# Performance work log

Hardware: AMD Instinct MI355X
Metric: run time of the kernel (lower is better)

Reference implementation:

```python
import jax, jax.numpy as jnp
import numpy as np

CONTEXT = 10  # symmetric_mask default; self.context is NOT used in call()
SCALE = 16.0  # hard-coded divisor in the source
NEG = 1e9


def setup_inputs() -> dict:
    key = jax.random.key(0)
    k1, k2, k3, k4 = jax.random.split(key, 4)
    B, N, D = 2, 4096, 512
    H, dh = 8, 64
    x = jax.random.normal(k1, (B, N, D), dtype=jnp.float32)
    Wq = jax.random.normal(k2, (H, D, dh), dtype=jnp.float32) * 1e-4
    Wv = jax.random.normal(k3, (H, D, dh), dtype=jnp.float32) * 1e-4
    Wup = jax.random.normal(k4, (H * dh, D), dtype=jnp.float32) * 1e-4
    return {"x": x, "Wq": Wq, "Wv": Wv, "Wup": Wup}


def reference(x, Wq, Wv, Wup):
    B, N, D = x.shape
    H, _, dh = Wq.shape
    # Per-head projections (no bias), vectorized over heads
    Q = jnp.einsum('bnd,hdk->bhnk', x, Wq)  # [B,H,N,dh]
    V = jnp.einsum('bnd,hdk->bhnk', x, Wv)  # [B,H,N,dh]
    # Full score matrix Q @ V^T / 16 (V doubles as keys in this module)
    scores = jnp.einsum('bhnk,bhmk->bhnm', Q, V) / SCALE  # [B,H,N,N]
    # Symmetric band mask: |i-j| <= CONTEXT and |i-j| > 0 (diagonal excluded)
    idx = jnp.arange(N)
    diff = jnp.abs(idx[:, None] - idx[None, :])
    mask = (diff <= CONTEXT) & (diff > 0)  # [N,N]
    scores = scores - NEG * (~mask).astype(scores.dtype)
    weights = jax.nn.softmax(scores, axis=-1)
    C = jnp.einsum('bhnm,bhmk->bhnk', weights, V)  # [B,H,N,dh]
    heads = C.transpose(0, 2, 1, 3).reshape(B, N, H * dh)  # concat heads
    return heads @ Wup  # [B,N,D]
```

## Files before the change

### kernel.cpp

```cpp
#include <hip/hip_runtime.h>
#include <math.h>

#define N_TOK 4096
#define DMODEL 512
#define NHEAD 8
#define DHEAD 64
#define CTX 10
#define NROW 8192

typedef __bf16 bf16x8 __attribute__((ext_vector_type(8)));
typedef float  f32x4  __attribute__((ext_vector_type(4)));

#define GLOAD_LDS16(g, l) __builtin_amdgcn_global_load_lds(                 \
    (const __attribute__((address_space(1))) void*)(g),                     \
    (__attribute__((address_space(3))) void*)(l), 16, 0, 0)

__global__ __launch_bounds__(256) void conv_x(const float* __restrict__ x,
                                              __bf16* __restrict__ xb)
{
    const int idx = (blockIdx.x * 256 + threadIdx.x) * 8;
    const float4 a = *(const float4*)(x + idx);
    const float4 b = *(const float4*)(x + idx + 4);
    bf16x8 o;
    o[0] = (__bf16)a.x; o[1] = (__bf16)a.y; o[2] = (__bf16)a.z; o[3] = (__bf16)a.w;
    o[4] = (__bf16)b.x; o[5] = (__bf16)b.y; o[6] = (__bf16)b.z; o[7] = (__bf16)b.w;
    *(bf16x8*)(xb + idx) = o;
}

__global__ __launch_bounds__(256) void conv_wqv(const float* __restrict__ Wq,
                                                const float* __restrict__ Wv,
                                                __bf16* __restrict__ Wt)
{
    __shared__ float T[64][65];
    const int k0  = blockIdx.x * 64;
    const int h   = blockIdx.y;
    const int mat = blockIdx.z;
    const float* src = (mat ? Wv : Wq) + (size_t)h * DMODEL * DHEAD;
    const int tid = threadIdx.x;
#pragma unroll
    for (int it = 0; it < 4; it++) {
        const int kr = it * 16 + (tid >> 4);
        const int c4 = (tid & 15) * 4;
        const float4 v = *(const float4*)(src + (size_t)(k0 + kr) * DHEAD + c4);
        T[kr][c4 + 0] = v.x; T[kr][c4 + 1] = v.y;
        T[kr][c4 + 2] = v.z; T[kr][c4 + 3] = v.w;
    }
    __syncthreads();
    const int c   = tid >> 2;
    const int kk0 = (tid & 3) * 16;
    __bf16* dst = Wt + (size_t)(mat * 512 + h * 64 + c) * DMODEL + k0 + kk0;
    bf16x8 o0, o1;
#pragma unroll
    for (int j = 0; j < 8; j++) o0[j] = (__bf16)T[kk0 + j][c];
#pragma unroll
    for (int j = 0; j < 8; j++) o1[j] = (__bf16)T[kk0 + 8 + j][c];
    *(bf16x8*)dst = o0;
    *(bf16x8*)(dst + 8) = o1;
}

__global__ __launch_bounds__(256) void conv_wup(const float* __restrict__ Wup,
                                                __bf16* __restrict__ Wt)
{
    __shared__ float T[64][65];
    const int k0 = blockIdx.x * 64;
    const int n0 = blockIdx.y * 64;
    const int tid = threadIdx.x;
#pragma unroll
    for (int it = 0; it < 4; it++) {
        const int kr = it * 16 + (tid >> 4);
        const int c4 = (tid & 15) * 4;
        const float4 v = *(const float4*)(Wup + (size_t)(k0 + kr) * DMODEL + n0 + c4);
        T[kr][c4 + 0] = v.x; T[kr][c4 + 1] = v.y;
        T[kr][c4 + 2] = v.z; T[kr][c4 + 3] = v.w;
    }
    __syncthreads();
    const int c   = tid >> 2;
    const int kk0 = (tid & 3) * 16;
    __bf16* dst = Wt + (size_t)(n0 + c) * DMODEL + k0 + kk0;
    bf16x8 o0, o1;
#pragma unroll
    for (int j = 0; j < 8; j++) o0[j] = (__bf16)T[kk0 + j][c];
#pragma unroll
    for (int j = 0; j < 8; j++) o1[j] = (__bf16)T[kk0 + 8 + j][c];
    *(bf16x8*)dst = o0;
    *(bf16x8*)(dst + 8) = o1;
}

__global__ __launch_bounds__(256) void gemm_qv_mfma(
    const __bf16* __restrict__ Xb,
    const __bf16* __restrict__ Wt,
    float* __restrict__ Qt,
    float* __restrict__ Vt)
{
    __shared__ __align__(16) __bf16 As[128 * 32];
    __shared__ __align__(16) __bf16 Bs[128 * 32];

    const int tid  = threadIdx.x;
    const int w    = tid >> 6;
    const int lane = tid & 63;
    const int lm   = lane & 15;
    const int q    = lane >> 4;
    const int wm   = w >> 1, wn = w & 1;
    const int row0 = blockIdx.y * 128;
    const int col0 = blockIdx.x * 128;

    const int sr = lane >> 2;
    const int sc = (lane & 3) * 8;
    const __bf16* gA0 = Xb + (size_t)(row0 + w * 32 +  0 + sr) * DMODEL + sc;
    const __bf16* gA1 = Xb + (size_t)(row0 + w * 32 + 16 + sr) * DMODEL + sc;
    const __bf16* gB0 = Wt + (size_t)(col0 + w * 32 +  0 + sr) * DMODEL + sc;
    const __bf16* gB1 = Wt + (size_t)(col0 + w * 32 + 16 + sr) * DMODEL + sc;
    __bf16* lA0 = As + (w * 32 +  0) * 32;
    __bf16* lA1 = As + (w * 32 + 16) * 32;
    __bf16* lB0 = Bs + (w * 32 +  0) * 32;
    __bf16* lB1 = Bs + (w * 32 + 16) * 32;

    f32x4 acc[4][4];
#pragma unroll
    for (int i = 0; i < 4; i++)
#pragma unroll
        for (int j = 0; j < 4; j++) acc[i][j] = (f32x4){0.f, 0.f, 0.f, 0.f};

    for (int k0 = 0; k0 < DMODEL; k0 += 32) {
        __syncthreads();
        GLOAD_LDS16(gA0, lA0); GLOAD_LDS16(gA1, lA1);
        GLOAD_LDS16(gB0, lB0); GLOAD_LDS16(gB1, lB1);
        gA0 += 32; gA1 += 32; gB0 += 32; gB1 += 32;
        __syncthreads();

        bf16x8 af[4], bfr[4];
#pragma unroll
        for (int mi = 0; mi < 4; mi++)
            af[mi] = *(const bf16x8*)&As[(wm * 64 + mi * 16 + lm) * 32 + q * 8];
#pragma unroll
        for (int ni = 0; ni < 4; ni++)
            bfr[ni] = *(const bf16x8*)&Bs[(wn * 64 + ni * 16 + lm) * 32 + q * 8];
#pragma unroll
        for (int mi = 0; mi < 4; mi++)
#pragma unroll
            for (int ni = 0; ni < 4; ni++)
                acc[mi][ni] = __builtin_amdgcn_mfma_f32_16x16x32_bf16(
                    af[mi], bfr[ni], acc[mi][ni], 0, 0, 0);
    }

#pragma unroll
    for (int ni = 0; ni < 4; ni++) {
        const int c  = col0 + wn * 64 + ni * 16 + lm;
        const int cc = c & 511;
        float* outB = (c < 512 ? Qt : Vt);
#pragma unroll
        for (int mi = 0; mi < 4; mi++) {
            const int m  = row0 + wm * 64 + mi * 16 + q * 4;
            const int bb = m >> 12;
            const int nt = m & (N_TOK - 1);
            *(f32x4*)(outB + ((size_t)(bb * 512 + cc)) * N_TOK + nt) = acc[mi][ni];
        }
    }
}

#define VSTRIDE 97
__global__ __launch_bounds__(256) void attn_band(
    const float* __restrict__ Qt,
    const float* __restrict__ Vt,
    __bf16* __restrict__ Hb16)
{
    __shared__ float Vs[64 * VSTRIDE];

    const int tid  = threadIdx.x;
    const int bh   = blockIdx.x >> 6;
    const int tile = blockIdx.x & 63;
    const int i0   = tile * 64;
    const int b    = bh >> 3;
    const int h    = bh & 7;

    const float* vband = Vt + (size_t)bh * DHEAD * N_TOK;
    const int tok0 = i0 - 12;
#pragma unroll
    for (int it = 0; it < 6; it++) {
        const int idx = it * 256 + tid;
        const int k   = idx / 24;
        const int s4  = idx - k * 24;
        const int tokg = tok0 + s4 * 4;
        const int tokc = min(max(tokg, 0), N_TOK - 4);
        const float4 v = *(const float4*)(vband + (size_t)k * N_TOK + tokc);
        float* dst = &Vs[k * VSTRIDE + s4 * 4];
        dst[0] = v.x; dst[1] = v.y; dst[2] = v.z; dst[3] = v.w;
    }

    const int lane = tid & 63;
    const int wv   = tid >> 6;
    const int il   = lane & 15;
    const int p    = lane >> 4;
    const int i    = i0 + wv * 16 + il;
    const int slot0 = wv * 16 + il + 2;

    const float* qbase = Qt + ((size_t)bh * DHEAD + p * 16) * N_TOK;
    float qv[16];
#pragma unroll
    for (int k = 0; k < 16; k++) qv[k] = qbase[(size_t)k * N_TOK + i];

    __syncthreads();

    float c[16];
#pragma unroll
    for (int k = 0; k < 16; k++) c[k] = 0.f;
    float Z = 0.f;

#pragma unroll 3
    for (int d = 0; d < 2 * CTX + 1; d++) {
        const float* vrow = &Vs[p * 16 * VSTRIDE + slot0 + d];
        float v[16];
#pragma unroll
        for (int k = 0; k < 16; k++) v[k] = vrow[k * VSTRIDE];
        float s = 0.f;
#pragma unroll
        for (int k = 0; k < 16; k++) s += qv[k] * v[k];
        s += __shfl_xor(s, 16, 64);
        s += __shfl_xor(s, 32, 64);

        const int j = i + d - CTX;
        const bool valid = (d != CTX) && (j >= 0) && (j < N_TOK);
        const float w = valid ? __expf(s * 0.0625f) : 0.f;
        Z += w;
#pragma unroll
        for (int k = 0; k < 16; k++) c[k] += w * v[k];
    }

    const float inv = 1.f / Z;
    __bf16* dst = Hb16 + ((size_t)(b * N_TOK + i)) * DMODEL + h * DHEAD + p * 16;
    bf16x8 o0, o1;
#pragma unroll
    for (int k = 0; k < 8; k++) o0[k] = (__bf16)(c[k] * inv);
#pragma unroll
    for (int k = 0; k < 8; k++) o1[k] = (__bf16)(c[8 + k] * inv);
    *(bf16x8*)dst = o0;
    *(bf16x8*)(dst + 8) = o1;
}

__global__ __launch_bounds__(256) void gemm_out_mfma(
    const __bf16* __restrict__ Hb,
    const __bf16* __restrict__ Wt,
    float* __restrict__ out)
{
    __shared__ __align__(16) __bf16 As[128 * 32];
    __shared__ __align__(16) __bf16 Bs[64 * 32];

    const int tid  = threadIdx.x;
    const int w    = tid >> 6;
    const int lane = tid & 63;
    const int lm   = lane & 15;
    const int q    = lane >> 4;
    const int row0 = blockIdx.y * 128;
    const int col0 = blockIdx.x * 64;

    const int sr = lane >> 2;
    const int sc = (lane & 3) * 8;
    const __bf16* gA0 = Hb + (size_t)(row0 + w * 32 +  0 + sr) * DMODEL + sc;
    const __bf16* gA1 = Hb + (size_t)(row0 + w * 32 + 16 + sr) * DMODEL + sc;
    const __bf16* gB0 = Wt + (size_t)(col0 + w * 16 + sr) * DMODEL + sc;
    __bf16* lA0 = As + (w * 32 +  0) * 32;
    __bf16* lA1 = As + (w * 32 + 16) * 32;
    __bf16* lB0 = Bs + (w * 16) * 32;

    f32x4 acc[2][4];
#pragma unroll
    for (int i = 0; i < 2; i++)
#pragma unroll
        for (int j = 0; j < 4; j++) acc[i][j] = (f32x4){0.f, 0.f, 0.f, 0.f};

    for (int k0 = 0; k0 < DMODEL; k0 += 32) {
        __syncthreads();
        GLOAD_LDS16(gA0, lA0); GLOAD_LDS16(gA1, lA1); GLOAD_LDS16(gB0, lB0);
        gA0 += 32; gA1 += 32; gB0 += 32;
        __syncthreads();

        bf16x8 af[2], bfr[4];
#pragma unroll
        for (int mi = 0; mi < 2; mi++)
            af[mi] = *(const bf16x8*)&As[(w * 32 + mi * 16 + lm) * 32 + q * 8];
#pragma unroll
        for (int ni = 0; ni < 4; ni++)
            bfr[ni] = *(const bf16x8*)&Bs[(ni * 16 + lm) * 32 + q * 8];
#pragma unroll
        for (int mi = 0; mi < 2; mi++)
#pragma unroll
            for (int ni = 0; ni < 4; ni++)
                acc[mi][ni] = __builtin_amdgcn_mfma_f32_16x16x32_bf16(
                    af[mi], bfr[ni], acc[mi][ni], 0, 0, 0);
    }

#pragma unroll
    for (int mi = 0; mi < 2; mi++) {
        const int m0 = row0 + w * 32 + mi * 16 + q * 4;
#pragma unroll
        for (int ni = 0; ni < 4; ni++) {
            const int n = col0 + ni * 16 + lm;
#pragma unroll
            for (int r = 0; r < 4; r++)
                out[(size_t)(m0 + r) * DMODEL + n] = acc[mi][ni][r];
        }
    }
}

extern "C" void kernel_launch(void* const* d_in, const int* in_sizes, int n_in,
                              void* d_out, int out_size, void* d_ws, size_t ws_size,
                              hipStream_t stream)
{
    const float* x   = (const float*)d_in[0];
    const float* Wq  = (const float*)d_in[1];
    const float* Wv  = (const float*)d_in[2];
    const float* Wup = (const float*)d_in[3];
    float* out = (float*)d_out;

    const size_t QV = (size_t)2 * NHEAD * N_TOK * DHEAD;
    float*  Qt   = (float*)d_ws;
    float*  Vt   = Qt + QV;
    __bf16* Xb   = (__bf16*)(Vt + QV);
    __bf16* Hb16 = Xb;
    __bf16* Wtqv = Xb + (size_t)NROW * DMODEL;
    __bf16* Wtup = Wtqv + (size_t)1024 * DMODEL;

    dim3 blk(256);
    conv_x   <<<dim3(2048),    blk, 0, stream>>>(x, Xb);
    conv_wqv <<<dim3(8, 8, 2), blk, 0, stream>>>(Wq, Wv, Wtqv);
    conv_wup <<<dim3(8, 8),    blk, 0, stream>>>(Wup, Wtup);
    gemm_qv_mfma <<<dim3(8, 64), blk, 0, stream>>>(Xb, Wtqv, Qt, Vt);
    attn_band    <<<dim3(1024),  blk, 0, stream>>>(Qt, Vt, Hb16);
    gemm_out_mfma<<<dim3(8, 64), blk, 0, stream>>>(Hb16, Wtup, out);
}
```

Before: 128.3 us.

## Fuse x bf16 conversion into QV GEMM and merge weight conversion kernels

The separate conv_x kernel is removed. The QV GEMM now loads fp32 x directly, converts it to bf16 in registers and stores it to LDS, replacing the async global-to-LDS copy for the A operand. The two weight-transpose kernels are merged into one launch of 192 blocks. This cuts two launches and a full bf16 round trip of x through memory. In exchange, each GEMM tile re-reads fp32 x, which is twice the bytes of bf16, and the A loads now pass through registers synchronously instead of via global_load_lds.

```diff
diff --git a/kernel.cpp b/kernel.cpp
--- a/kernel.cpp
+++ b/kernel.cpp
@@ -8,6 +8,7 @@
 #define CTX 10
 #define NROW 8192
 
+typedef __bf16 bf16x4 __attribute__((ext_vector_type(4)));
 typedef __bf16 bf16x8 __attribute__((ext_vector_type(8)));
 typedef float  f32x4  __attribute__((ext_vector_type(4)));
 
@@ -15,40 +16,54 @@
     (const __attribute__((address_space(1))) void*)(g),                     \
     (__attribute__((address_space(3))) void*)(l), 16, 0, 0)
 
-__global__ __launch_bounds__(256) void conv_x(const float* __restrict__ x,
-                                              __bf16* __restrict__ xb)
-{
-    const int idx = (blockIdx.x * 256 + threadIdx.x) * 8;
-    const float4 a = *(const float4*)(x + idx);
-    const float4 b = *(const float4*)(x + idx + 4);
-    bf16x8 o;
-    o[0] = (__bf16)a.x; o[1] = (__bf16)a.y; o[2] = (__bf16)a.z; o[3] = (__bf16)a.w;
-    o[4] = (__bf16)b.x; o[5] = (__bf16)b.y; o[6] = (__bf16)b.z; o[7] = (__bf16)b.w;
-    *(bf16x8*)(xb + idx) = o;
-}
-
-__global__ __launch_bounds__(256) void conv_wqv(const float* __restrict__ Wq,
-                                                const float* __restrict__ Wv,
-                                                __bf16* __restrict__ Wt)
+__global__ __launch_bounds__(256) void conv_w(const float* __restrict__ Wq,
+                                              const float* __restrict__ Wv,
+                                              const float* __restrict__ Wup,
+                                              __bf16* __restrict__ Wtqv,
+                                              __bf16* __restrict__ Wtup)
 {
     __shared__ float T[64][65];
-    const int k0  = blockIdx.x * 64;
-    const int h   = blockIdx.y;
-    const int mat = blockIdx.z;
-    const float* src = (mat ? Wv : Wq) + (size_t)h * DMODEL * DHEAD;
     const int tid = threadIdx.x;
+    const int bid = blockIdx.x;
+
+    const float* src;
+    __bf16* dstBase;
+    int k0, rowScale;
+    int rowBase;
+    int srcStride;
+    if (bid < 128) {
+        k0 = (bid & 7) * 64;
+        const int h   = (bid >> 3) & 7;
+        const int mat = bid >> 6;
+        src = (mat ? Wv : Wq) + (size_t)h * DMODEL * DHEAD;
+        dstBase = Wtqv;
+        rowBase = mat * 512 + h * 64;
+        srcStride = DHEAD;
+        rowScale = 1;
+    } else {
+        const int b2 = bid - 128;
+        k0 = (b2 & 7) * 64;
+        const int n0 = (b2 >> 3) * 64;
+        src = Wup + n0;
+        dstBase = Wtup;
+        rowBase = n0;
+        srcStride = DMODEL;
+        rowScale = 1;
+    }
+    (void)rowScale;
+
 #pragma unroll
     for (int it = 0; it < 4; it++) {
         const int kr = it * 16 + (tid >> 4);
         const int c4 = (tid & 15) * 4;
-        const float4 v = *(const float4*)(src + (size_t)(k0 + kr) * DHEAD + c4);
+        const float4 v = *(const float4*)(src + (size_t)(k0 + kr) * srcStride + c4);
         T[kr][c4 + 0] = v.x; T[kr][c4 + 1] = v.y;
         T[kr][c4 + 2] = v.z; T[kr][c4 + 3] = v.w;
     }
     __syncthreads();
     const int c   = tid >> 2;
     const int kk0 = (tid & 3) * 16;
-    __bf16* dst = Wt + (size_t)(mat * 512 + h * 64 + c) * DMODEL + k0 + kk0;
+    __bf16* dst = dstBase + (size_t)(rowBase + c) * DMODEL + k0 + kk0;
     bf16x8 o0, o1;
 #pragma unroll
     for (int j = 0; j < 8; j++) o0[j] = (__bf16)T[kk0 + j][c];
@@ -58,36 +73,8 @@
     *(bf16x8*)(dst + 8) = o1;
 }
 
-__global__ __launch_bounds__(256) void conv_wup(const float* __restrict__ Wup,
-                                                __bf16* __restrict__ Wt)
-{
-    __shared__ float T[64][65];
-    const int k0 = blockIdx.x * 64;
-    const int n0 = blockIdx.y * 64;
-    const int tid = threadIdx.x;
-#pragma unroll
-    for (int it = 0; it < 4; it++) {
-        const int kr = it * 16 + (tid >> 4);
-        const int c4 = (tid & 15) * 4;
-        const float4 v = *(const float4*)(Wup + (size_t)(k0 + kr) * DMODEL + n0 + c4);
-        T[kr][c4 + 0] = v.x; T[kr][c4 + 1] = v.y;
-        T[kr][c4 + 2] = v.z; T[kr][c4 + 3] = v.w;
-    }
-    __syncthreads();
-    const int c   = tid >> 2;
-    const int kk0 = (tid & 3) * 16;
-    __bf16* dst = Wt + (size_t)(n0 + c) * DMODEL + k0 + kk0;
-    bf16x8 o0, o1;
-#pragma unroll
-    for (int j = 0; j < 8; j++) o0[j] = (__bf16)T[kk0 + j][c];
-#pragma unroll
-    for (int j = 0; j < 8; j++) o1[j] = (__bf16)T[kk0 + 8 + j][c];
-    *(bf16x8*)dst = o0;
-    *(bf16x8*)(dst + 8) = o1;
-}
-
 __global__ __launch_bounds__(256) void gemm_qv_mfma(
-    const __bf16* __restrict__ Xb,
+    const float* __restrict__ x,
     const __bf16* __restrict__ Wt,
     float* __restrict__ Qt,
     float* __restrict__ Vt)
@@ -104,14 +91,14 @@
     const int row0 = blockIdx.y * 128;
     const int col0 = blockIdx.x * 128;
 
+    const int asr = tid >> 3;
+    const int asc = (tid & 7) * 4;
+    const float* gA = x + (size_t)(row0 + asr) * DMODEL + asc;
+
     const int sr = lane >> 2;
     const int sc = (lane & 3) * 8;
-    const __bf16* gA0 = Xb + (size_t)(row0 + w * 32 +  0 + sr) * DMODEL + sc;
-    const __bf16* gA1 = Xb + (size_t)(row0 + w * 32 + 16 + sr) * DMODEL + sc;
     const __bf16* gB0 = Wt + (size_t)(col0 + w * 32 +  0 + sr) * DMODEL + sc;
     const __bf16* gB1 = Wt + (size_t)(col0 + w * 32 + 16 + sr) * DMODEL + sc;
-    __bf16* lA0 = As + (w * 32 +  0) * 32;
-    __bf16* lA1 = As + (w * 32 + 16) * 32;
     __bf16* lB0 = Bs + (w * 32 +  0) * 32;
     __bf16* lB1 = Bs + (w * 32 + 16) * 32;
 
@@ -122,10 +109,22 @@
         for (int j = 0; j < 4; j++) acc[i][j] = (f32x4){0.f, 0.f, 0.f, 0.f};
 
     for (int k0 = 0; k0 < DMODEL; k0 += 32) {
+        float4 a[4];
+#pragma unroll
+        for (int p = 0; p < 4; p++)
+            a[p] = *(const float4*)(gA + (size_t)p * 32 * DMODEL);
+        gA += 32;
+
         __syncthreads();
-        GLOAD_LDS16(gA0, lA0); GLOAD_LDS16(gA1, lA1);
+#pragma unroll
+        for (int p = 0; p < 4; p++) {
+            bf16x4 o;
+            o[0] = (__bf16)a[p].x; o[1] = (__bf16)a[p].y;
+            o[2] = (__bf16)a[p].z; o[3] = (__bf16)a[p].w;
+            *(bf16x4*)&As[(asr + p * 32) * 32 + asc] = o;
+        }
         GLOAD_LDS16(gB0, lB0); GLOAD_LDS16(gB1, lB1);
-        gA0 += 32; gA1 += 32; gB0 += 32; gB1 += 32;
+        gB0 += 32; gB1 += 32;
         __syncthreads();
 
         bf16x8 af[4], bfr[4];
@@ -315,16 +314,13 @@
     const size_t QV = (size_t)2 * NHEAD * N_TOK * DHEAD;
     float*  Qt   = (float*)d_ws;
     float*  Vt   = Qt + QV;
-    __bf16* Xb   = (__bf16*)(Vt + QV);
-    __bf16* Hb16 = Xb;
-    __bf16* Wtqv = Xb + (size_t)NROW * DMODEL;
+    __bf16* Hb16 = (__bf16*)(Vt + QV);
+    __bf16* Wtqv = Hb16 + (size_t)NROW * DMODEL;
     __bf16* Wtup = Wtqv + (size_t)1024 * DMODEL;
 
     dim3 blk(256);
-    conv_x   <<<dim3(2048),    blk, 0, stream>>>(x, Xb);
-    conv_wqv <<<dim3(8, 8, 2), blk, 0, stream>>>(Wq, Wv, Wtqv);
-    conv_wup <<<dim3(8, 8),    blk, 0, stream>>>(Wup, Wtup);
-    gemm_qv_mfma <<<dim3(8, 64), blk, 0, stream>>>(Xb, Wtqv, Qt, Vt);
+    conv_w       <<<dim3(192),   blk, 0, stream>>>(Wq, Wv, Wup, Wtqv, Wtup);
+    gemm_qv_mfma <<<dim3(8, 64), blk, 0, stream>>>(x, Wtqv, Qt, Vt);
     attn_band    <<<dim3(1024),  blk, 0, stream>>>(Qt, Vt, Hb16);
     gemm_out_mfma<<<dim3(8, 64), blk, 0, stream>>>(Hb16, Wtup, out);
 }
```

New measurement: 126.9 us. About the same (-1.1%).
